# Performance work log

Hardware: AMD Instinct MI355X
Metric: run time of the kernel (lower is better)

Reference implementation:

```python
import jax, jax.numpy as jnp
import numpy as np

NOISE_LEVEL = 0.05  # midpoint of uniform(0.01, 0.1) in the original
A_COEF = 0.99
B_COEF = 0.01


def setup_inputs() -> dict:
    key = jax.random.key(0)
    k1, k2 = jax.random.split(key)
    C, T = 256, 220500
    waveform = jax.random.normal(k1, (C, T), dtype=jnp.float32)
    white_noise = jax.random.normal(k2, (C, T), dtype=jnp.float32)
    return {"waveform": waveform, "white_noise": white_noise}


def _pink_noise(white_noise):
    # First-order IIR: f[0] = w[0]; f[i] = 0.99*f[i-1] + 0.01*w[i]
    # Vectorized over channels, lax.scan over time.
    w0 = white_noise[:, 0]                      # [C]
    wt = white_noise[:, 1:].T                   # [T-1, C]

    def step(carry, w_t):
        f = A_COEF * carry + B_COEF * w_t
        return f, f

    _, rest = jax.lax.scan(step, w0, wt)        # rest: [T-1, C]
    pink = jnp.concatenate([w0[None, :], rest], axis=0).T  # [C, T]
    return pink


def reference(waveform, white_noise):
    pink = _pink_noise(white_noise)
    mixed = waveform + pink * NOISE_LEVEL
    max_val = jnp.max(jnp.abs(mixed))
    # normalize only if peak exceeds 1.0
    return jnp.where(max_val > 1.0, mixed / max_val, mixed)
```

## Files before the change

kernel.cpp:

```cpp
#include <hip/hip_runtime.h>


#define TLEN 220500
#define CHANNELS 256

constexpr int CHK  = 8192;
constexpr int PL   = 512;
constexpr int NP   = CHK / PL;
constexpr int NCH  = 27;
constexpr int NWAVES = NCH * CHANNELS;
constexpr int NB   = NWAVES / 4;

constexpr float AC = 0.99f;
constexpr float BC = 0.01f;
constexpr float NL = 0.05f;

constexpr double dpow(double a, long n) { double r = 1.0; for (long i = 0; i < n; ++i) r *= a; return r; }

constexpr float S8P0 = (float)dpow(0.99, 8);
constexpr float S8P1 = (float)dpow(0.99, 16);
constexpr float S8P2 = (float)dpow(0.99, 32);
constexpr float S8P3 = (float)dpow(0.99, 64);
constexpr float S8P4 = (float)dpow(0.99, 128);
constexpr float S8P5 = (float)dpow(0.99, 256);
constexpr float A512 = (float)dpow(0.99, 512);
constexpr float L2A8 = -0.11599655756609923f;

__device__ __forceinline__ float wave_scan8(float f, int lane) {
    { float o = __shfl_up(f, 1,  64); if (lane >= 1)  f = fmaf(S8P0, o, f); }
    { float o = __shfl_up(f, 2,  64); if (lane >= 2)  f = fmaf(S8P1, o, f); }
    { float o = __shfl_up(f, 4,  64); if (lane >= 4)  f = fmaf(S8P2, o, f); }
    { float o = __shfl_up(f, 8,  64); if (lane >= 8)  f = fmaf(S8P3, o, f); }
    { float o = __shfl_up(f, 16, 64); if (lane >= 16) f = fmaf(S8P4, o, f); }
    { float o = __shfl_up(f, 32, 64); if (lane >= 32) f = fmaf(S8P5, o, f); }
    return f;
}

__device__ __forceinline__ float serial8(const float4& a, const float4& b) {
    float f = BC * a.x;
    f = fmaf(AC, f, BC * a.y);
    f = fmaf(AC, f, BC * a.z);
    f = fmaf(AC, f, BC * a.w);
    f = fmaf(AC, f, BC * b.x);
    f = fmaf(AC, f, BC * b.y);
    f = fmaf(AC, f, BC * b.z);
    f = fmaf(AC, f, BC * b.w);
    return f;
}

__global__ void init_max_kernel(unsigned int* gmax) { *gmax = 0u; }

template <int USE_ATOMIC>
__global__ __launch_bounds__(256)
void fused_kernel(const float* __restrict__ waveform,
                  const float* __restrict__ white,
                  float* __restrict__ out,
                  unsigned int* __restrict__ gmax,
                  float* __restrict__ blockmax)
{
    __shared__ float sM[4];
    const int tid  = threadIdx.x;
    const int lane = tid & 63;
    const int wv   = tid >> 6;
    const int W    = blockIdx.x * 4 + wv;
    const int ch   = W / NCH;
    const int chunk = W - ch * NCH;
    const size_t row = (size_t)ch * TLEN;
    const float* __restrict__ wrow = white + row;
    const float* __restrict__ arow = waveform + row;
    float* __restrict__ orow = out + row;
    const int c0 = chunk * CHK;
    const int l8 = 8 * lane;
    const float D8L = __builtin_exp2f((float)lane * L2A8);

    float4 wu0, wu1, wu2, wu3;
    if (chunk > 0) {
        const float* wb = wrow + (c0 - 1024) + l8;
        wu0 = *reinterpret_cast<const float4*>(wb);
        wu1 = *reinterpret_cast<const float4*>(wb + 4);
        wu2 = *reinterpret_cast<const float4*>(wb + 512);
        wu3 = *reinterpret_cast<const float4*>(wb + 516);
    }

    float4 WA[3], WB[3], AA[3], AB[3];
    const float4 z4 = make_float4(0.f, 0.f, 0.f, 0.f);

    auto LDP = [&](int p, float4& wa, float4& wb, float4& aa, float4& ab) {
        const int g = c0 + p * PL + l8;
        wa = z4; wb = z4; aa = z4; ab = z4;
        if (g < TLEN) {
            wa = *reinterpret_cast<const float4*>(wrow + g);
            aa = *reinterpret_cast<const float4*>(arow + g);
        }
        if (g + 4 < TLEN) {
            wb = *reinterpret_cast<const float4*>(wrow + g + 4);
            ab = *reinterpret_cast<const float4*>(arow + g + 4);
        }
    };

    LDP(0, WA[0], WB[0], AA[0], AB[0]);
    LDP(1, WA[1], WB[1], AA[1], AB[1]);

    float E = 0.f;
    if (chunk > 0) {
        float f = serial8(wu0, wu1);
        float p = wave_scan8(f, lane);
        E = __shfl(p, 63, 64);
        f = serial8(wu2, wu3);
        p = wave_scan8(f, lane);
        E = fmaf(A512, E, __shfl(p, 63, 64));
    } else {
        E = __shfl(WA[0].x, 0, 64);
    }

    float mx = 0.f;
    #pragma unroll
    for (int p = 0; p < NP; ++p) {
        const int s  = p % 3;
        const int s2 = (p + 2) % 3;
        if (p + 2 < NP)
            LDP(p + 2, WA[s2], WB[s2], AA[s2], AB[s2]);

        float f  = serial8(WA[s], WB[s]);
        float pb = wave_scan8(f, lane);
        float e  = __shfl_up(pb, 1, 64);
        if (lane == 0) e = 0.f;
        const float T = __shfl(pb, 63, 64);

        float fst = fmaf(D8L, E, e);
        float4 ma, mb;
        fst = fmaf(AC, fst, BC * WA[s].x); ma.x = fmaf(NL, fst, AA[s].x);
        fst = fmaf(AC, fst, BC * WA[s].y); ma.y = fmaf(NL, fst, AA[s].y);
        fst = fmaf(AC, fst, BC * WA[s].z); ma.z = fmaf(NL, fst, AA[s].z);
        fst = fmaf(AC, fst, BC * WA[s].w); ma.w = fmaf(NL, fst, AA[s].w);
        fst = fmaf(AC, fst, BC * WB[s].x); mb.x = fmaf(NL, fst, AB[s].x);
        fst = fmaf(AC, fst, BC * WB[s].y); mb.y = fmaf(NL, fst, AB[s].y);
        fst = fmaf(AC, fst, BC * WB[s].z); mb.z = fmaf(NL, fst, AB[s].z);
        fst = fmaf(AC, fst, BC * WB[s].w); mb.w = fmaf(NL, fst, AB[s].w);

        const int g = c0 + p * PL + l8;
        if (g < TLEN) {
            *reinterpret_cast<float4*>(orow + g) = ma;
            mx = fmaxf(mx, fmaxf(fmaxf(fabsf(ma.x), fabsf(ma.y)),
                                 fmaxf(fabsf(ma.z), fabsf(ma.w))));
        }
        if (g + 4 < TLEN) {
            *reinterpret_cast<float4*>(orow + g + 4) = mb;
            mx = fmaxf(mx, fmaxf(fmaxf(fabsf(mb.x), fabsf(mb.y)),
                                 fmaxf(fabsf(mb.z), fabsf(mb.w))));
        }
        E = fmaf(A512, E, T);
    }

    #pragma unroll
    for (int d = 32; d >= 1; d >>= 1)
        mx = fmaxf(mx, __shfl_xor(mx, d, 64));
    if (lane == 0) sM[wv] = mx;
    __syncthreads();
    if (tid == 0) {
        float m = fmaxf(fmaxf(sM[0], sM[1]), fmaxf(sM[2], sM[3]));
        if (USE_ATOMIC) {
            atomicMax(gmax, __float_as_uint(m));
        } else {
            blockmax[blockIdx.x] = m;
        }
    }
}

__global__ __launch_bounds__(256)
void reduce_max_kernel(const float* __restrict__ blockmax, unsigned int* __restrict__ gmax)
{
    __shared__ float sM[4];
    const int tid  = threadIdx.x;
    const int lane = tid & 63;
    const int wv   = tid >> 6;
    float mx = 0.f;
    for (int i = tid; i < NB; i += 256)
        mx = fmaxf(mx, blockmax[i]);
    #pragma unroll
    for (int d = 32; d >= 1; d >>= 1)
        mx = fmaxf(mx, __shfl_xor(mx, d, 64));
    if (lane == 0) sM[wv] = mx;
    __syncthreads();
    if (tid == 0)
        *gmax = __float_as_uint(fmaxf(fmaxf(sM[0], sM[1]), fmaxf(sM[2], sM[3])));
}

__global__ __launch_bounds__(256)
void scale_kernel(float* __restrict__ out, const unsigned int* __restrict__ gmax, int n4)
{
    const float m = __uint_as_float(*gmax);
    const float s = (m > 1.0f) ? (1.0f / m) : 1.0f;
    float4* p = reinterpret_cast<float4*>(out);
    int i = blockIdx.x * blockDim.x + threadIdx.x;
    const int stride = gridDim.x * blockDim.x;
    for (; i < n4; i += stride) {
        float4 v = p[i];
        v.x *= s; v.y *= s; v.z *= s; v.w *= s;
        p[i] = v;
    }
}

extern "C" void kernel_launch(void* const* d_in, const int* in_sizes, int n_in,
                              void* d_out, int out_size, void* d_ws, size_t ws_size,
                              hipStream_t stream)
{
    const float* waveform = (const float*)d_in[0];
    const float* white    = (const float*)d_in[1];
    float* out            = (float*)d_out;

    unsigned int* gmax = (unsigned int*)d_ws;
    float* blockmax    = (float*)((char*)d_ws + 256);
    const bool ws_ok   = ws_size >= 256 + (size_t)NB * sizeof(float);

    const int n4 = out_size / 4;

    if (ws_ok) {
        hipLaunchKernelGGL((fused_kernel<0>), dim3(NB), dim3(256), 0, stream,
                           waveform, white, out, gmax, blockmax);
        hipLaunchKernelGGL(reduce_max_kernel, dim3(1), dim3(256), 0, stream,
                           blockmax, gmax);
    } else {
        hipLaunchKernelGGL(init_max_kernel, dim3(1), dim3(1), 0, stream, gmax);
        hipLaunchKernelGGL((fused_kernel<1>), dim3(NB), dim3(256), 0, stream,
                           waveform, white, out, gmax, blockmax);
    }
    hipLaunchKernelGGL(scale_kernel, dim3(3072), dim3(256), 0, stream,
                       out, gmax, n4);
}
```

Baseline: 255.2 us.

## Shrink scan segments to 2048 with a 512-sample warm-up and nontemporal loads

```diff
diff --git a/kernel.cpp b/kernel.cpp
--- a/kernel.cpp
+++ b/kernel.cpp
@@ -4,12 +4,11 @@
 #define TLEN 220500
 #define CHANNELS 256
 
-constexpr int CHK  = 8192;
-constexpr int PL   = 512;
-constexpr int NP   = CHK / PL;
-constexpr int NCH  = 27;
-constexpr int NWAVES = NCH * CHANNELS;
-constexpr int NB   = NWAVES / 4;
+constexpr int SEGL = 2048;
+constexpr int WUP  = 512;
+constexpr int SPC  = (TLEN + SEGL - 1) / SEGL;
+constexpr int NSEG = SPC * CHANNELS;
+constexpr int NB   = NSEG / 4;
 
 constexpr float AC = 0.99f;
 constexpr float BC = 0.01f;
@@ -26,6 +25,15 @@
 constexpr float A512 = (float)dpow(0.99, 512);
 constexpr float L2A8 = -0.11599655756609923f;
 
+typedef float f4 __attribute__((ext_vector_type(4)));
+
+__device__ __forceinline__ f4 ntld4(const float* p) {
+    return __builtin_nontemporal_load(reinterpret_cast<const f4*>(p));
+}
+__device__ __forceinline__ void ntst4(float* p, f4 v) {
+    __builtin_nontemporal_store(v, reinterpret_cast<f4*>(p));
+}
+
 __device__ __forceinline__ float wave_scan8(float f, int lane) {
     { float o = __shfl_up(f, 1,  64); if (lane >= 1)  f = fmaf(S8P0, o, f); }
     { float o = __shfl_up(f, 2,  64); if (lane >= 2)  f = fmaf(S8P1, o, f); }
@@ -36,7 +44,7 @@
     return f;
 }
 
-__device__ __forceinline__ float serial8(const float4& a, const float4& b) {
+__device__ __forceinline__ float serial8(const f4& a, const f4& b) {
     float f = BC * a.x;
     f = fmaf(AC, f, BC * a.y);
     f = fmaf(AC, f, BC * a.z);
@@ -62,94 +70,83 @@
     const int tid  = threadIdx.x;
     const int lane = tid & 63;
     const int wv   = tid >> 6;
-    const int W    = blockIdx.x * 4 + wv;
-    const int ch   = W / NCH;
-    const int chunk = W - ch * NCH;
+    const int S    = blockIdx.x * 4 + wv;
+    const int ch   = S / SPC;
+    const int s    = S - ch * SPC;
     const size_t row = (size_t)ch * TLEN;
     const float* __restrict__ wrow = white + row;
     const float* __restrict__ arow = waveform + row;
     float* __restrict__ orow = out + row;
-    const int c0 = chunk * CHK;
-    const int l8 = 8 * lane;
+    const int seg0 = s * SEGL;
+    const int l8   = 8 * lane;
     const float D8L = __builtin_exp2f((float)lane * L2A8);
-
-    float4 wu0, wu1, wu2, wu3;
-    if (chunk > 0) {
-        const float* wb = wrow + (c0 - 1024) + l8;
-        wu0 = *reinterpret_cast<const float4*>(wb);
-        wu1 = *reinterpret_cast<const float4*>(wb + 4);
-        wu2 = *reinterpret_cast<const float4*>(wb + 512);
-        wu3 = *reinterpret_cast<const float4*>(wb + 516);
-    }
-
-    float4 WA[3], WB[3], AA[3], AB[3];
-    const float4 z4 = make_float4(0.f, 0.f, 0.f, 0.f);
-
-    auto LDP = [&](int p, float4& wa, float4& wb, float4& aa, float4& ab) {
-        const int g = c0 + p * PL + l8;
-        wa = z4; wb = z4; aa = z4; ab = z4;
+    const f4 z4 = {0.f, 0.f, 0.f, 0.f};
+
+    f4 wu0 = z4, wu1 = z4;
+    if (s > 0) {
+        const float* wb = wrow + (seg0 - WUP) + l8;
+        wu0 = ntld4(wb);
+        wu1 = ntld4(wb + 4);
+    }
+    f4 Wa[4], Wb[4], Aa[4], Ab[4];
+    #pragma unroll
+    for (int p = 0; p < 4; ++p) {
+        const int g = seg0 + p * 512 + l8;
+        Wa[p] = z4; Wb[p] = z4; Aa[p] = z4; Ab[p] = z4;
         if (g < TLEN) {
-            wa = *reinterpret_cast<const float4*>(wrow + g);
-            aa = *reinterpret_cast<const float4*>(arow + g);
+            Wa[p] = ntld4(wrow + g);
+            Aa[p] = ntld4(arow + g);
         }
         if (g + 4 < TLEN) {
-            wb = *reinterpret_cast<const float4*>(wrow + g + 4);
-            ab = *reinterpret_cast<const float4*>(arow + g + 4);
-        }
-    };
-
-    LDP(0, WA[0], WB[0], AA[0], AB[0]);
-    LDP(1, WA[1], WB[1], AA[1], AB[1]);
-
-    float E = 0.f;
-    if (chunk > 0) {
+            Wb[p] = ntld4(wrow + g + 4);
+            Ab[p] = ntld4(arow + g + 4);
+        }
+    }
+
+    float Tw = 0.f;
+    if (s > 0) {
         float f = serial8(wu0, wu1);
         float p = wave_scan8(f, lane);
-        E = __shfl(p, 63, 64);
-        f = serial8(wu2, wu3);
-        p = wave_scan8(f, lane);
-        E = fmaf(A512, E, __shfl(p, 63, 64));
-    } else {
-        E = __shfl(WA[0].x, 0, 64);
-    }
+        Tw = __shfl(p, 63, 64);
+    }
+    float eB[4], T[4];
+    #pragma unroll
+    for (int p = 0; p < 4; ++p) {
+        float f  = serial8(Wa[p], Wb[p]);
+        float sc = wave_scan8(f, lane);
+        float ex = __shfl_up(sc, 1, 64);
+        eB[p] = (lane == 0) ? 0.f : ex;
+        T[p]  = __shfl(sc, 63, 64);
+    }
+
+    float E = (s > 0) ? Tw : __shfl(Wa[0].x, 0, 64);
 
     float mx = 0.f;
     #pragma unroll
-    for (int p = 0; p < NP; ++p) {
-        const int s  = p % 3;
-        const int s2 = (p + 2) % 3;
-        if (p + 2 < NP)
-            LDP(p + 2, WA[s2], WB[s2], AA[s2], AB[s2]);
-
-        float f  = serial8(WA[s], WB[s]);
-        float pb = wave_scan8(f, lane);
-        float e  = __shfl_up(pb, 1, 64);
-        if (lane == 0) e = 0.f;
-        const float T = __shfl(pb, 63, 64);
-
-        float fst = fmaf(D8L, E, e);
-        float4 ma, mb;
-        fst = fmaf(AC, fst, BC * WA[s].x); ma.x = fmaf(NL, fst, AA[s].x);
-        fst = fmaf(AC, fst, BC * WA[s].y); ma.y = fmaf(NL, fst, AA[s].y);
-        fst = fmaf(AC, fst, BC * WA[s].z); ma.z = fmaf(NL, fst, AA[s].z);
-        fst = fmaf(AC, fst, BC * WA[s].w); ma.w = fmaf(NL, fst, AA[s].w);
-        fst = fmaf(AC, fst, BC * WB[s].x); mb.x = fmaf(NL, fst, AB[s].x);
-        fst = fmaf(AC, fst, BC * WB[s].y); mb.y = fmaf(NL, fst, AB[s].y);
-        fst = fmaf(AC, fst, BC * WB[s].z); mb.z = fmaf(NL, fst, AB[s].z);
-        fst = fmaf(AC, fst, BC * WB[s].w); mb.w = fmaf(NL, fst, AB[s].w);
-
-        const int g = c0 + p * PL + l8;
+    for (int p = 0; p < 4; ++p) {
+        float f = fmaf(D8L, E, eB[p]);
+        f4 ma, mb;
+        f = fmaf(AC, f, BC * Wa[p].x); ma.x = fmaf(NL, f, Aa[p].x);
+        f = fmaf(AC, f, BC * Wa[p].y); ma.y = fmaf(NL, f, Aa[p].y);
+        f = fmaf(AC, f, BC * Wa[p].z); ma.z = fmaf(NL, f, Aa[p].z);
+        f = fmaf(AC, f, BC * Wa[p].w); ma.w = fmaf(NL, f, Aa[p].w);
+        f = fmaf(AC, f, BC * Wb[p].x); mb.x = fmaf(NL, f, Ab[p].x);
+        f = fmaf(AC, f, BC * Wb[p].y); mb.y = fmaf(NL, f, Ab[p].y);
+        f = fmaf(AC, f, BC * Wb[p].z); mb.z = fmaf(NL, f, Ab[p].z);
+        f = fmaf(AC, f, BC * Wb[p].w); mb.w = fmaf(NL, f, Ab[p].w);
+
+        const int g = seg0 + p * 512 + l8;
         if (g < TLEN) {
-            *reinterpret_cast<float4*>(orow + g) = ma;
+            *reinterpret_cast<f4*>(orow + g) = ma;
             mx = fmaxf(mx, fmaxf(fmaxf(fabsf(ma.x), fabsf(ma.y)),
                                  fmaxf(fabsf(ma.z), fabsf(ma.w))));
         }
         if (g + 4 < TLEN) {
-            *reinterpret_cast<float4*>(orow + g + 4) = mb;
+            *reinterpret_cast<f4*>(orow + g + 4) = mb;
             mx = fmaxf(mx, fmaxf(fmaxf(fabsf(mb.x), fabsf(mb.y)),
                                  fmaxf(fabsf(mb.z), fabsf(mb.w))));
         }
-        E = fmaf(A512, E, T);
+        E = fmaf(A512, E, T[p]);
     }
 
     #pragma unroll
@@ -191,13 +188,13 @@
 {
     const float m = __uint_as_float(*gmax);
     const float s = (m > 1.0f) ? (1.0f / m) : 1.0f;
-    float4* p = reinterpret_cast<float4*>(out);
+    f4* p = reinterpret_cast<f4*>(out);
     int i = blockIdx.x * blockDim.x + threadIdx.x;
     const int stride = gridDim.x * blockDim.x;
     for (; i < n4; i += stride) {
-        float4 v = p[i];
+        f4 v = p[i];
         v.x *= s; v.y *= s; v.z *= s; v.w *= s;
-        p[i] = v;
+        __builtin_nontemporal_store(v, &p[i]);
     }
 }
 
```

Result: no change. 259.5 us (+1.7%).
